# Kernel tuning notes

Measured on AMD Instinct MI355X. Metric: run time of the kernel, lower is better.

## Reference

```python
import jax, jax.numpy as jnp
import numpy as np

N, E, F_IN, HID, HEADS, NCLS, NG = 50000, 800000, 128, 128, 4, 10, 512
C = HID // HEADS          # per-head channels
BN_EPS = 1e-5
NEG_SLOPE = 0.2           # SuperGATConv default negative_slope
N_CONV = 3


def setup_inputs() -> dict:
    key = jax.random.key(0)
    ks = jax.random.split(key, 16)
    x = jax.random.normal(ks[0], (N, F_IN), jnp.float32)
    # edges with no self loops (reference appends self loops itself, as SuperGATConv does)
    src = jax.random.randint(ks[1], (E,), 0, N, dtype=jnp.int32)
    off = jax.random.randint(ks[2], (E,), 1, N, dtype=jnp.int32)
    dst = (src + off) % N
    edge_index = jnp.stack([src, dst], axis=0)
    batch = jnp.sort(jax.random.randint(ks[3], (N,), 0, NG, dtype=jnp.int32))
    s = 0.1
    # BatchNorm params per module init: weight=1, bias=1e-4 (running stats fresh: mean=0, var=1)
    inp = {
        "x": x, "edge_index": edge_index, "batch": batch,
        "bn_feat_g": jnp.ones((F_IN,), jnp.float32), "bn_feat_b": jnp.full((F_IN,), 1e-4, jnp.float32),
        "w_feat": jax.random.normal(ks[4], (F_IN, HID), jnp.float32) * s,
        "b_feat": jnp.zeros((HID,), jnp.float32),
        "bn_conv_g": jnp.ones((N_CONV, HID), jnp.float32), "bn_conv_b": jnp.full((N_CONV, HID), 1e-4, jnp.float32),
        "w_gat": jax.random.normal(ks[5], (N_CONV, HID, HID), jnp.float32) * s,
        "att_l": jax.random.normal(ks[6], (N_CONV, HEADS, C), jnp.float32) * s,
        "att_r": jax.random.normal(ks[7], (N_CONV, HEADS, C), jnp.float32) * s,
        "b_gat": jnp.zeros((N_CONV, HID), jnp.float32),
        "bn_fc_g": jnp.ones((HID,), jnp.float32), "bn_fc_b": jnp.full((HID,), 1e-4, jnp.float32),
        "w_fc": jax.random.normal(ks[8], (HID, HID), jnp.float32) * s,
        "b_fc": jnp.zeros((HID,), jnp.float32),
        "bn_hid_g": jnp.ones((HID,), jnp.float32), "bn_hid_b": jnp.full((HID,), 1e-4, jnp.float32),
        "w_cls": jax.random.normal(ks[9], (HID, NCLS), jnp.float32) * s,
        "b_cls": jnp.zeros((NCLS,), jnp.float32),
    }
    return inp


def _bn_eval(h, g, b):
    # eval-mode BatchNorm1d with fresh running stats (mean=0, var=1)
    return h * (g / jnp.sqrt(1.0 + BN_EPS)) + b


def _segment_softmax(a, seg, num_segments):
    # softmax over edges grouped by destination node (PyG softmax semantics)
    m = jax.ops.segment_max(a, seg, num_segments=num_segments)
    a = jnp.exp(a - m[seg])
    s = jax.ops.segment_sum(a, seg, num_segments=num_segments)
    return a / (s[seg] + 1e-16)


def _supergat_mx(h, src, dst, W, att_l, att_r, bias):
    # h: [N, HID] -> per-head features [N, H, C]
    hh = (h @ W).reshape(N, HEADS, C)
    h_j = hh[src]  # source (message) features  [E2, H, C]
    h_i = hh[dst]  # destination features       [E2, H, C]
    logits = jnp.einsum('ehc,ehc->eh', h_i, h_j)                       # MX dot-product
    alpha = jnp.einsum('ehc,hc->eh', h_j, att_l) + jnp.einsum('ehc,hc->eh', h_i, att_r)
    alpha = alpha * jax.nn.sigmoid(logits)
    alpha = jax.nn.leaky_relu(alpha, NEG_SLOPE)
    alpha = _segment_softmax(alpha, dst, N)                            # [E2, H]
    out = jax.ops.segment_sum(h_j * alpha[..., None], dst, num_segments=N)
    return out.reshape(N, HID) + bias


def reference(x, edge_index, batch, bn_feat_g, bn_feat_b, w_feat, b_feat,
              bn_conv_g, bn_conv_b, w_gat, att_l, att_r, b_gat,
              bn_fc_g, bn_fc_b, w_fc, b_fc, bn_hid_g, bn_hid_b, w_cls, b_cls):
    loops = jnp.arange(N, dtype=edge_index.dtype)
    src = jnp.concatenate([edge_index[0], loops])   # SuperGATConv adds self loops
    dst = jnp.concatenate([edge_index[1], loops])
    h = _bn_eval(x, bn_feat_g, bn_feat_b)
    h = jax.nn.relu(h @ w_feat + b_feat)            # GCNConv(gfn=True) == Linear
    for i in range(N_CONV):
        h = _bn_eval(h, bn_conv_g[i], bn_conv_b[i])
        h = jax.nn.relu(_supergat_mx(h, src, dst, w_gat[i], att_l[i], att_r[i], b_gat[i]))
    g = jax.ops.segment_sum(h, batch, num_segments=NG)  # global_add_pool -> [NG, HID]
    g = _bn_eval(g, bn_fc_g, bn_fc_b)
    g = jax.nn.relu(g @ w_fc + b_fc)
    g = _bn_eval(g, bn_hid_g, bn_hid_b)
    logits = g @ w_cls + b_cls
    att_loss = jnp.float32(0.0)  # eval mode: no edge-sampled attention loss
    return jax.nn.log_softmax(logits, axis=-1), att_loss
```

## Files before the change

### kernel.cpp

```cpp
#include <hip/hip_runtime.h>

#define NN 50000
#define EE 800000
#define FHID 128
#define NHEAD 4
#define NGRAPH 512
#define NCLS 10
#define BK 256
#define BCH 2048
#define NBLK_E 391
#define NBUCK 196
#define CAPB 6144

typedef unsigned short u16;
typedef unsigned int u32;
typedef unsigned long long u64;
typedef __attribute__((ext_vector_type(8))) short bf16x8;
typedef __attribute__((ext_vector_type(4))) float f32x4;
typedef __attribute__((ext_vector_type(2))) float f32x2;

__device__ __forceinline__ float bf2f(u16 u){
    union { u32 i; float f; } v; v.i = ((u32)u) << 16; return v.f;
}
__device__ __forceinline__ float bflo(u32 u){
    union { u32 i; float f; } v; v.i = u << 16; return v.f;
}
__device__ __forceinline__ float bfhi(u32 u){
    union { u32 i; float f; } v; v.i = u & 0xffff0000u; return v.f;
}
__device__ __forceinline__ u16 f2bf(float f){
    union { float f; u32 i; } v; v.f = f;
    u32 r = v.i + 0x7fffu + ((v.i >> 16) & 1u);
    return (u16)(r >> 16);
}
__device__ __forceinline__ u32 pack2(float a, float b){
    return ((u32)f2bf(b) << 16) | f2bf(a);
}
__device__ __forceinline__ float loadF(const void* p, int i, int isf32){
    return isf32 ? ((const float*)p)[i] : bf2f(((const u16*)p)[i]);
}
__device__ __forceinline__ void unpk8(uint4 v, float* f){
    f[0]=bflo(v.x); f[1]=bfhi(v.x);
    f[2]=bflo(v.y); f[3]=bfhi(v.y);
    f[4]=bflo(v.z); f[5]=bfhi(v.z);
    f[6]=bflo(v.w); f[7]=bfhi(v.w);
}
__device__ __forceinline__ void unpk8v(uint4 v, f32x2* h){
    h[0] = (f32x2){bflo(v.x), bfhi(v.x)};
    h[1] = (f32x2){bflo(v.y), bfhi(v.y)};
    h[2] = (f32x2){bflo(v.z), bfhi(v.z)};
    h[3] = (f32x2){bflo(v.w), bfhi(v.w)};
}

__device__ __forceinline__ float quad_red(float x){
    int t0 = __builtin_amdgcn_mov_dpp(__float_as_int(x), 0xB1, 0xF, 0xF, true);
    float y = x + __int_as_float(t0);
    int t1 = __builtin_amdgcn_mov_dpp(__float_as_int(y), 0x4E, 0xF, 0xF, true);
    return y + __int_as_float(t1);
}

__device__ int detect_local(const u16* x, int tid, int nthreads, int* lds){
    int ok = 0;
    for (int i = tid; i < 1024; i += nthreads){
        u16 u = x[i];
        int e = (u >> 7) & 0xFF;
        if ((u & 0x7fff) == 0 || (e >= 0x70 && e <= 0x85)) ok++;
    }
    lds[tid] = ok;
    __syncthreads();
    for (int o2 = nthreads >> 1; o2 > 0; o2 >>= 1){
        if (tid < o2) lds[tid] += lds[tid + o2];
        __syncthreads();
    }
    int r = (lds[0] < 900) ? 1 : 0;
    __syncthreads();
    return r;
}

__global__ __launch_bounds__(256) void prep_all(
        const u16* __restrict__ xz,
        const void* w_feat, const void* b_feat, const void* bn_feat_g, const void* bn_feat_b,
        const void* w_gat, const void* bn_conv_g, const void* bn_conv_b, const void* b_gat,
        const void* wfc, const void* bfc, const void* bnfg, const void* bnfb,
        const void* bnhg, const void* bnhb, const void* wcls, const void* bcls,
        const void* attl, const void* attr,
        u16* __restrict__ Wt, float* __restrict__ cvec, float* __restrict__ biasv,
        float* __restrict__ hp, int* __restrict__ dflag, int* __restrict__ gcur)
{
    __shared__ int ldsi[256];
    __shared__ float red[128];
    int bid = blockIdx.x, t = threadIdx.x;
    int isf32 = detect_local(xz, t, 256, ldsi);
    if (bid == 0){
        if (t == 0) dflag[0] = isf32;
        gcur[t] = t * CAPB;
    }

    if (bid < 512){
        if (t >= 128) return;
        int L = bid >> 7;
        int n = bid & 127;
        int k = t;
        const float rs = rsqrtf(1.0f + 1e-5f);
        float wv, bg, bb;
        if (L == 0){
            wv = loadF(w_feat, k*FHID + n, isf32);
            bg = loadF(bn_feat_g, k, isf32);
            bb = loadF(bn_feat_b, k, isf32);
        } else {
            wv = loadF(w_gat, (L-1)*FHID*FHID + k*FHID + n, isf32);
            bg = loadF(bn_conv_g, (L-1)*FHID + k, isf32);
            bb = loadF(bn_conv_b, (L-1)*FHID + k, isf32);
        }
        Wt[L*FHID*FHID + n*FHID + k] = f2bf(bg * rs * wv);
        red[k] = bb * wv;
        __syncthreads();
        for (int o2 = 64; o2 > 0; o2 >>= 1){
            if (k < o2) red[k] += red[k + o2];
            __syncthreads();
        }
        if (k == 0){
            float c = red[0];
            if (L == 0) c += loadF(b_feat, n, isf32);
            cvec[L*FHID + n] = c;
            if (L > 0) biasv[L*FHID + n] = loadF(b_gat, (L-1)*FHID + n, isf32);
        }
    } else {
        int gt = (bid - 512)*256 + t;
        for (int i = gt; i < FHID*FHID; i += 16*256) hp[i] = loadF(wfc, i, isf32);
        if (gt < FHID*NCLS) hp[16384 + gt] = loadF(wcls, gt, isf32);
        if (gt >= 2048 && gt < 2048 + 3*FHID){
            int i = gt - 2048;
            hp[18320 + i] = loadF(attl, i, isf32);
            hp[18704 + i] = loadF(attr, i, isf32);
        }
        if (gt >= 2560 && gt < 2560 + FHID){
            int tt = gt - 2560;
            hp[17664 + tt] = loadF(bnfg, tt, isf32);
            hp[17792 + tt] = loadF(bnfb, tt, isf32);
            hp[17920 + tt] = loadF(bfc,  tt, isf32);
            hp[18048 + tt] = loadF(bnhg, tt, isf32);
            hp[18176 + tt] = loadF(bnhb, tt, isf32);
        }
        if (gt >= 3072 && gt < 3072 + NCLS) hp[18304 + (gt - 3072)] = loadF(bcls, gt - 3072, isf32);
    }
}

__global__ __launch_bounds__(256) void gemm128(const void* __restrict__ A,
                                               const u16* __restrict__ Wt,
                                               const float* __restrict__ cvec,
                                               u16* __restrict__ out, int relu,
                                               int araw, const int* __restrict__ flag,
                                               const float* __restrict__ attl,
                                               const float* __restrict__ attr,
                                               float* __restrict__ al,
                                               float* __restrict__ ar)
{
    int wave = threadIdx.x >> 6;
    int lane = threadIdx.x & 63;
    int m = lane & 15, quad = lane >> 4;
    int row = blockIdx.x * 64 + wave * 16 + m;
    bool v0 = row < NN;
    bool f32in = araw && flag[0];
    const u16*  Au = (const u16*)A;
    const float* Af = (const float*)A;
    f32x4 acc[8];
#pragma unroll
    for (int j = 0; j < 8; j++) acc[j] = (f32x4){0.f,0.f,0.f,0.f};
#pragma unroll
    for (int t = 0; t < 4; t++){
        bf16x8 a0 = {0,0,0,0,0,0,0,0};
        int kof = t*32 + quad*8;
        if (f32in){
            if (v0){
                const float* p = Af + (size_t)row*FHID + kof;
                float4 u0 = *(const float4*)p, u1 = *(const float4*)(p+4);
                a0[0]=(short)f2bf(u0.x); a0[1]=(short)f2bf(u0.y);
                a0[2]=(short)f2bf(u0.z); a0[3]=(short)f2bf(u0.w);
                a0[4]=(short)f2bf(u1.x); a0[5]=(short)f2bf(u1.y);
                a0[6]=(short)f2bf(u1.z); a0[7]=(short)f2bf(u1.w);
            }
        } else {
            if (v0) a0 = *(const bf16x8*)(Au + (size_t)row*FHID + kof);
        }
#pragma unroll
        for (int ct = 0; ct < 8; ct++){
            bf16x8 wfrag = *(const bf16x8*)(Wt + (ct*16 + m)*FHID + kof);
            acc[ct] = __builtin_amdgcn_mfma_f32_16x16x32_bf16(wfrag, a0, acc[ct], 0, 0, 0);
        }
    }
    bool doa = (attl != nullptr);
    float sl[4] = {0.f,0.f,0.f,0.f};
    float sr[4] = {0.f,0.f,0.f,0.f};
#pragma unroll
    for (int ct = 0; ct < 8; ct++){
        int cb = ct*16 + quad*4;
        float4 cv = *(const float4*)(cvec + cb);
        float w0 = acc[ct][0] + cv.x;
        float w1 = acc[ct][1] + cv.y;
        float w2 = acc[ct][2] + cv.z;
        float w3 = acc[ct][3] + cv.w;
        if (relu){
            w0 = fmaxf(w0, 0.f); w1 = fmaxf(w1, 0.f);
            w2 = fmaxf(w2, 0.f); w3 = fmaxf(w3, 0.f);
        }
        if (doa){
            int h = ct >> 1;
            float4 tl = *(const float4*)(attl + cb);
            float4 tr = *(const float4*)(attr + cb);
            sl[h] += w0*tl.x + w1*tl.y + w2*tl.z + w3*tl.w;
            sr[h] += w0*tr.x + w1*tr.y + w2*tr.z + w3*tr.w;
        }
        if (v0){
            uint2 st; st.x = pack2(w0, w1); st.y = pack2(w2, w3);
            *(uint2*)(out + (size_t)row*FHID + cb) = st;
        }
    }
    if (doa){
#pragma unroll
        for (int h = 0; h < 4; h++){
            sl[h] += __shfl_xor(sl[h], 16, 64);
            sl[h] += __shfl_xor(sl[h], 32, 64);
            sr[h] += __shfl_xor(sr[h], 16, 64);
            sr[h] += __shfl_xor(sr[h], 32, 64);
        }
        if (v0){
            al[row*NHEAD + quad] = sl[quad];
            ar[row*NHEAD + quad] = sr[quad];
        }
    }
}

__global__ __launch_bounds__(256) void bin_edges(const int* __restrict__ srcp,
        const int* __restrict__ dstp, int* __restrict__ gcur, u64* __restrict__ binned)
{
    __shared__ int h[BK], lb[BK], gb[BK], cur[BK];
    __shared__ u64 stage[BCH];
    int t = threadIdx.x;
    h[t] = 0;
    __syncthreads();
    int base = blockIdx.x * BCH;
    int sv[8], dv[8];
#pragma unroll
    for (int k = 0; k < 8; k++){
        int e = base + k*256 + t;
        int d = -1, s = 0;
        if (e < EE){
            d = dstp[e]; s = srcp[e];
            if ((u32)d >= NN) d = -1;
        }
        sv[k] = s; dv[k] = d;
        if (d >= 0) atomicAdd(&h[d >> 8], 1);
    }
    __syncthreads();
    lb[t] = h[t];
    __syncthreads();
    for (int off = 1; off < BK; off <<= 1){
        int x = (t >= off) ? lb[t - off] : 0;
        __syncthreads();
        lb[t] += x;
        __syncthreads();
    }
    int excl = lb[t] - h[t];
    int tot  = lb[BK-1];
    __syncthreads();
    lb[t] = excl;
    gb[t] = h[t] ? atomicAdd(&gcur[t], h[t]) : 0;
    cur[t] = 0;
    __syncthreads();
#pragma unroll
    for (int k = 0; k < 8; k++){
        int d = dv[k];
        if (d >= 0){
            int b = d >> 8;
            int p = lb[b] + atomicAdd(&cur[b], 1);
            stage[p] = ((u64)(u32)d << 32) | (u32)sv[k];
        }
    }
    __syncthreads();
    for (int i = t; i < tot; i += 256){
        u64 pr = stage[i];
        int b = (int)(pr >> 40);
        binned[gb[b] + (i - lb[b])] = pr;
    }
}

__global__ __launch_bounds__(512) void build_csr(const u64* __restrict__ binned,
        const int* __restrict__ gcur, int2* __restrict__ rowdeg, int* __restrict__ colbuf)
{
    __shared__ int deg[BK], ls[BK], cur[BK];
    __shared__ int colstage[CAPB];
    int b = blockIdx.x, t = threadIdx.x;
    int gb = b * CAPB;
    int cnt = gcur[b] - gb;
    if (cnt < 0) cnt = 0;
    if (cnt > CAPB) cnt = CAPB;
    if (t < BK) deg[t] = 0;
    __syncthreads();
    for (int i = t; i < cnt; i += 512){
        int d = (int)(binned[gb + i] >> 32);
        atomicAdd(&deg[d & 255], 1);
    }
    __syncthreads();
    if (t < BK) ls[t] = deg[t];
    __syncthreads();
    for (int off = 1; off < BK; off <<= 1){
        int x = (t < BK && t >= off) ? ls[t - off] : 0;
        __syncthreads();
        if (t < BK) ls[t] += x;
        __syncthreads();
    }
    if (t < BK){
        int excl = ls[t] - deg[t];
        int node = b*256 + t;
        if (node < NN) rowdeg[node] = (int2){gb + excl, gb + excl + deg[t]};
        cur[t] = excl;
    }
    __syncthreads();
    for (int i = t; i < cnt; i += 512){
        u64 pr = binned[gb + i];
        int d = (int)(pr >> 32) & 255;
        int s = (int)(u32)pr;
        int p = atomicAdd(&cur[d], 1);
        colstage[p] = s;
    }
    __syncthreads();
    for (int i = t; i < cnt; i += 512) colbuf[gb + i] = colstage[i];
}

__device__ __forceinline__ void load_e(uint4& X, float& F, int e, int e1,
        const int* __restrict__ colbuf, const u16* __restrict__ hh,
        const float* __restrict__ al, int chbase, int head)
{
    int si = colbuf[e];
    bool bad = (e >= e1) || ((u32)si >= NN);
    if (bad) si = 0;
    X = *(const uint4*)(hh + (size_t)si*FHID + chbase);
    float f = al[si*NHEAD + head];
    F = bad ? -1e30f : f;
}

__device__ __forceinline__ void comp_e(uint4 X, float F,
        const f32x2* hd2, float arn, float& s, f32x2* o2)
{
    f32x2 hs2[4]; unpk8v(X, hs2);
    f32x2 d2 = hd2[0]*hs2[0];
    d2 = hd2[1]*hs2[1] + d2;
    d2 = hd2[2]*hs2[2] + d2;
    d2 = hd2[3]*hs2[3] + d2;
    float lg = quad_red(d2[0] + d2[1]);
    float a2 = (F + arn) * (1.0f / (1.0f + __expf(-lg)));
    a2 = fmaxf(a2, 0.2f*a2);
    float pe = __expf(fminf(a2, 60.f));
    s += pe;
    f32x2 pe2 = (f32x2){pe, pe};
    o2[0] = pe2*hs2[0] + o2[0];
    o2[1] = pe2*hs2[1] + o2[1];
    o2[2] = pe2*hs2[2] + o2[2];
    o2[3] = pe2*hs2[3] + o2[3];
}

__global__ __launch_bounds__(256, 8) void supergat_conv(const u16* __restrict__ hh,
        const float* __restrict__ al, const float* __restrict__ ar,
        const int2* __restrict__ rowdeg, const int* __restrict__ colbuf,
        const float* __restrict__ bias, u16* __restrict__ hout)
{
    int node = (blockIdx.x*256 + threadIdx.x) >> 6;
    int lane = threadIdx.x & 63;
    int group = lane >> 4;
    int gl    = lane & 15;
    int head  = gl >> 2;
    int chbase = head*32 + (gl & 3)*8;
    if (node >= NN) return;

    uint4 hdv = *(const uint4*)(hh + (size_t)node*FHID + chbase);
    f32x2 hd2[4]; unpk8v(hdv, hd2);
    float arn = ar[node*NHEAD + head];
    float aln = al[node*NHEAD + head];

    f32x2 dd2 = hd2[0]*hd2[0];
    dd2 = hd2[1]*hd2[1] + dd2;
    dd2 = hd2[2]*hd2[2] + dd2;
    dd2 = hd2[3]*hd2[3] + dd2;
    float d = quad_red(dd2[0] + dd2[1]);
    float a = (aln + arn) * (1.0f / (1.0f + __expf(-d)));
    a = fmaxf(a, 0.2f*a);
    float p = __expf(fminf(a, 60.f));
    if (group != 0) p = 0.f;
    float s = p;
    f32x2 p2 = (f32x2){p, p};
    f32x2 o2[4];
    o2[0] = p2*hd2[0];
    o2[1] = p2*hd2[1];
    o2[2] = p2*hd2[2];
    o2[3] = p2*hd2[3];

    int2 rd = rowdeg[node];
    int e0 = rd.x, e1 = rd.y;
    if (e0 < 0) e0 = 0;
    if (e1 > BK*CAPB) e1 = BK*CAPB;
    int it = (e1 - e0 + 3) >> 2;
    int e = e0 + group;

    if (it > 0){
        uint4 xA, xB; float fA, fB;
        load_e(xA, fA, e, e1, colbuf, hh, al, chbase, head);
        e += 4;
        while (true){
            if (it == 1){ comp_e(xA, fA, hd2, arn, s, o2); break; }
            load_e(xB, fB, e, e1, colbuf, hh, al, chbase, head); e += 4;
            comp_e(xA, fA, hd2, arn, s, o2);
            --it;
            if (it == 1){ comp_e(xB, fB, hd2, arn, s, o2); break; }
            load_e(xA, fA, e, e1, colbuf, hh, al, chbase, head); e += 4;
            comp_e(xB, fB, hd2, arn, s, o2);
            --it;
        }
    }

    s += __shfl_xor(s, 16, 64);
    s += __shfl_xor(s, 32, 64);
#pragma unroll
    for (int i = 0; i < 4; i++){
        float x0 = o2[i][0], x1 = o2[i][1];
        x0 += __shfl_xor(x0, 16, 64);
        x0 += __shfl_xor(x0, 32, 64);
        x1 += __shfl_xor(x1, 16, 64);
        x1 += __shfl_xor(x1, 32, 64);
        o2[i] = (f32x2){x0, x1};
    }

    if (group == 0){
        float inv = 1.0f / (s + 1e-16f);
        uint4 w;
        w.x = pack2(fmaxf(o2[0][0]*inv + bias[chbase+0], 0.f),
                    fmaxf(o2[0][1]*inv + bias[chbase+1], 0.f));
        w.y = pack2(fmaxf(o2[1][0]*inv + bias[chbase+2], 0.f),
                    fmaxf(o2[1][1]*inv + bias[chbase+3], 0.f));
        w.z = pack2(fmaxf(o2[2][0]*inv + bias[chbase+4], 0.f),
                    fmaxf(o2[2][1]*inv + bias[chbase+5], 0.f));
        w.w = pack2(fmaxf(o2[3][0]*inv + bias[chbase+6], 0.f),
                    fmaxf(o2[3][1]*inv + bias[chbase+7], 0.f));
        *(uint4*)(hout + (size_t)node*FHID + chbase) = w;
    }
}

__global__ void pool_head(const u16* __restrict__ h, const int* __restrict__ batch,
                          const float* __restrict__ hp, const int* __restrict__ flag,
                          void* __restrict__ out)
{
    __shared__ int bounds[2];
    __shared__ float gb[FHID];
    __shared__ float g2[FHID];
    __shared__ float lg[16];
    int gi = blockIdx.x, t = threadIdx.x;
    int isf32 = flag[0];
    if (t < 2){
        int target = gi + t;
        int lo = 0, hi = NN;
        while (lo < hi){
            int mid = (lo + hi) >> 1;
            if (batch[mid] < target) lo = mid + 1; else hi = mid;
        }
        bounds[t] = lo;
    }
    __syncthreads();
    float s0 = 0.f, s1 = 0.f, s2 = 0.f, s3 = 0.f;
    int node = bounds[0], nend = bounds[1];
    for (; node + 3 < nend; node += 4){
        s0 += bf2f(h[(size_t)(node+0)*FHID + t]);
        s1 += bf2f(h[(size_t)(node+1)*FHID + t]);
        s2 += bf2f(h[(size_t)(node+2)*FHID + t]);
        s3 += bf2f(h[(size_t)(node+3)*FHID + t]);
    }
    for (; node < nend; node++) s0 += bf2f(h[(size_t)node*FHID + t]);
    float acc0 = (s0 + s1) + (s2 + s3);
    const float rs = rsqrtf(1.0f + 1e-5f);
    gb[t] = acc0 * (hp[17664 + t] * rs) + hp[17792 + t];
    __syncthreads();
    float acc = hp[17920 + t];
    for (int k = 0; k < FHID; k++) acc += gb[k] * hp[k*FHID + t];
    acc = fmaxf(acc, 0.f);
    g2[t] = acc * (hp[18048 + t] * rs) + hp[18176 + t];
    __syncthreads();
    if (t < NCLS){
        float l = hp[18304 + t];
        for (int k = 0; k < FHID; k++) l += g2[k] * hp[16384 + k*NCLS + t];
        lg[t] = l;
    }
    __syncthreads();
    if (t == 0){
        float mx = lg[0];
        for (int j = 1; j < NCLS; j++) mx = fmaxf(mx, lg[j]);
        float se = 0.f;
        for (int j = 0; j < NCLS; j++) se += __expf(lg[j] - mx);
        float lse = logf(se) + mx;
        if (isf32){
            float* o = (float*)out;
            for (int j = 0; j < NCLS; j++) o[gi*NCLS + j] = lg[j] - lse;
            if (gi == 0) o[NGRAPH*NCLS] = 0.f;
        } else {
            u16* o = (u16*)out;
            for (int j = 0; j < NCLS; j++) o[gi*NCLS + j] = f2bf(lg[j] - lse);
            if (gi == 0) o[NGRAPH*NCLS] = 0;
        }
    }
}

extern "C" void kernel_launch(void* const* d_in, const int* in_sizes, int n_in,
                              void* d_out, int out_size, void* d_ws, size_t ws_size,
                              hipStream_t stream)
{
    (void)in_sizes; (void)n_in; (void)out_size; (void)ws_size;
    const void* x         = d_in[0];
    const int* edge       = (const int*)d_in[1];
    const int* batch      = (const int*)d_in[2];

    char* ws = (char*)d_ws;
    size_t off = 0;
    auto alloc = [&](size_t bytes) -> char* {
        char* p = ws + off; off += (bytes + 255) & ~(size_t)255; return p;
    };
    int*   dflag   = (int*)  alloc(256);
    u16*   WtAll   = (u16*)  alloc((size_t)4*FHID*FHID*2);
    float* cvecAll = (float*)alloc((size_t)4*FHID*4);
    float* biasv   = (float*)alloc((size_t)4*FHID*4);
    float* headp   = (float*)alloc((size_t)19088*4);
    float* al      = (float*)alloc((size_t)NN*NHEAD*4);
    float* ar      = (float*)alloc((size_t)NN*NHEAD*4);
    int*   gcur    = (int*)  alloc((size_t)BK*4);
    int2*  rowdeg  = (int2*) alloc((size_t)NN*8);
    int*   colbuf  = (int*)  alloc((size_t)(BK*CAPB + 64)*4);
    u16*   hA      = (u16*)  alloc((size_t)NN*FHID*2);
    u16*   hB      = (u16*)  alloc((size_t)NN*FHID*2);
    u64*   binned  = (u64*)hB;

    const int* srcp = edge;
    const int* dstp = edge + EE;

    prep_all<<<528, 256, 0, stream>>>((const u16*)x,
        d_in[5], d_in[6], d_in[3], d_in[4], d_in[9], d_in[7], d_in[8], d_in[12],
        d_in[15], d_in[16], d_in[13], d_in[14], d_in[17], d_in[18], d_in[19], d_in[20],
        d_in[10], d_in[11],
        WtAll, cvecAll, biasv, headp, dflag, gcur);

    bin_edges<<<NBLK_E, 256, 0, stream>>>(srcp, dstp, gcur, binned);
    build_csr<<<NBUCK, 512, 0, stream>>>(binned, gcur, rowdeg, colbuf);

    gemm128<<<(NN + 63)/64, 256, 0, stream>>>(x, WtAll, cvecAll, hA, 1, 1, dflag,
                                              nullptr, nullptr, nullptr, nullptr);

    for (int i = 0; i < 3; i++){
        gemm128<<<(NN + 63)/64, 256, 0, stream>>>(hA, WtAll + (i+1)*FHID*FHID,
                                                  cvecAll + (i+1)*FHID, hB, 0, 0, dflag,
                                                  headp + 18320 + i*FHID,
                                                  headp + 18704 + i*FHID, al, ar);
        supergat_conv<<<(NN + 3)/4, 256, 0, stream>>>(hB, al, ar, rowdeg, colbuf,
                                                      biasv + (i+1)*FHID, hA);
    }

    pool_head<<<NGRAPH, 128, 0, stream>>>(hA, batch, headp, dflag, d_out);
}
```

Before: 380.8 us.

## Merge prep with edge binning and CSR build with first GEMM; widen pool head

Independent stages now share one launch each. Parameter prep and edge binning run as one grid, split by block index. CSR construction and the first feature GEMM also run as one grid. The gcur bucket cursors are now zeroed with a memset, so binning no longer waits for prep. The pooling/head kernel moves to 512 threads, splitting the node sum and the FC matvec across four sub-groups. This cuts launch count and fills idle CUs during small serial stages, at the cost of higher shared-memory use per block in the merged kernels.

```diff
diff --git a/kernel.cpp b/kernel.cpp
--- a/kernel.cpp
+++ b/kernel.cpp
@@ -11,6 +11,7 @@
 #define NBLK_E 391
 #define NBUCK 196
 #define CAPB 6144
+#define NBLK_G 782
 
 typedef unsigned short u16;
 typedef unsigned int u32;
@@ -39,12 +40,6 @@
 __device__ __forceinline__ float loadF(const void* p, int i, int isf32){
     return isf32 ? ((const float*)p)[i] : bf2f(((const u16*)p)[i]);
 }
-__device__ __forceinline__ void unpk8(uint4 v, float* f){
-    f[0]=bflo(v.x); f[1]=bfhi(v.x);
-    f[2]=bflo(v.y); f[3]=bfhi(v.y);
-    f[4]=bflo(v.z); f[5]=bfhi(v.z);
-    f[6]=bflo(v.w); f[7]=bfhi(v.w);
-}
 __device__ __forceinline__ void unpk8v(uint4 v, f32x2* h){
     h[0] = (f32x2){bflo(v.x), bfhi(v.x)};
     h[1] = (f32x2){bflo(v.y), bfhi(v.y)};
@@ -77,7 +72,7 @@
     return r;
 }
 
-__global__ __launch_bounds__(256) void prep_all(
+__device__ __forceinline__ void prep_body(int bid, int t,
         const u16* __restrict__ xz,
         const void* w_feat, const void* b_feat, const void* bn_feat_g, const void* bn_feat_b,
         const void* w_gat, const void* bn_conv_g, const void* bn_conv_b, const void* b_gat,
@@ -85,16 +80,12 @@
         const void* bnhg, const void* bnhb, const void* wcls, const void* bcls,
         const void* attl, const void* attr,
         u16* __restrict__ Wt, float* __restrict__ cvec, float* __restrict__ biasv,
-        float* __restrict__ hp, int* __restrict__ dflag, int* __restrict__ gcur)
+        float* __restrict__ hp, int* __restrict__ dflag)
 {
     __shared__ int ldsi[256];
     __shared__ float red[128];
-    int bid = blockIdx.x, t = threadIdx.x;
     int isf32 = detect_local(xz, t, 256, ldsi);
-    if (bid == 0){
-        if (t == 0) dflag[0] = isf32;
-        gcur[t] = t * CAPB;
-    }
+    if (bid == 0 && t == 0) dflag[0] = isf32;
 
     if (bid < 512){
         if (t >= 128) return;
@@ -146,20 +137,92 @@
     }
 }
 
-__global__ __launch_bounds__(256) void gemm128(const void* __restrict__ A,
-                                               const u16* __restrict__ Wt,
-                                               const float* __restrict__ cvec,
-                                               u16* __restrict__ out, int relu,
-                                               int araw, const int* __restrict__ flag,
-                                               const float* __restrict__ attl,
-                                               const float* __restrict__ attr,
-                                               float* __restrict__ al,
-                                               float* __restrict__ ar)
-{
-    int wave = threadIdx.x >> 6;
-    int lane = threadIdx.x & 63;
+__device__ __forceinline__ void bin_body(int bid, int t,
+        const int* __restrict__ srcp, const int* __restrict__ dstp,
+        int* __restrict__ gcur, u64* __restrict__ binned)
+{
+    __shared__ int h[BK], lb[BK], gbs[BK], cur[BK];
+    __shared__ u64 stage[BCH];
+    h[t] = 0;
+    __syncthreads();
+    int base = bid * BCH;
+    int sv[8], dv[8];
+#pragma unroll
+    for (int k = 0; k < 8; k++){
+        int e = base + k*256 + t;
+        int d = -1, s = 0;
+        if (e < EE){
+            d = dstp[e]; s = srcp[e];
+            if ((u32)d >= NN) d = -1;
+        }
+        sv[k] = s; dv[k] = d;
+        if (d >= 0) atomicAdd(&h[d >> 8], 1);
+    }
+    __syncthreads();
+    lb[t] = h[t];
+    __syncthreads();
+    for (int off = 1; off < BK; off <<= 1){
+        int x = (t >= off) ? lb[t - off] : 0;
+        __syncthreads();
+        lb[t] += x;
+        __syncthreads();
+    }
+    int excl = lb[t] - h[t];
+    int tot  = lb[BK-1];
+    __syncthreads();
+    lb[t] = excl;
+    gbs[t] = t*CAPB + (h[t] ? atomicAdd(&gcur[t], h[t]) : 0);
+    cur[t] = 0;
+    __syncthreads();
+#pragma unroll
+    for (int k = 0; k < 8; k++){
+        int d = dv[k];
+        if (d >= 0){
+            int b = d >> 8;
+            int p = lb[b] + atomicAdd(&cur[b], 1);
+            stage[p] = ((u64)(u32)d << 32) | (u32)sv[k];
+        }
+    }
+    __syncthreads();
+    for (int i = t; i < tot; i += 256){
+        u64 pr = stage[i];
+        int b = (int)(pr >> 40);
+        binned[gbs[b] + (i - lb[b])] = pr;
+    }
+}
+
+__global__ __launch_bounds__(256) void prep_bin(
+        const u16* __restrict__ xz,
+        const void* w_feat, const void* b_feat, const void* bn_feat_g, const void* bn_feat_b,
+        const void* w_gat, const void* bn_conv_g, const void* bn_conv_b, const void* b_gat,
+        const void* wfc, const void* bfc, const void* bnfg, const void* bnfb,
+        const void* bnhg, const void* bnhb, const void* wcls, const void* bcls,
+        const void* attl, const void* attr,
+        u16* __restrict__ Wt, float* __restrict__ cvec, float* __restrict__ biasv,
+        float* __restrict__ hp, int* __restrict__ dflag,
+        const int* __restrict__ srcp, const int* __restrict__ dstp,
+        int* __restrict__ gcur, u64* __restrict__ binned)
+{
+    if (blockIdx.x < 528){
+        prep_body(blockIdx.x, threadIdx.x, xz, w_feat, b_feat, bn_feat_g, bn_feat_b,
+                  w_gat, bn_conv_g, bn_conv_b, b_gat, wfc, bfc, bnfg, bnfb,
+                  bnhg, bnhb, wcls, bcls, attl, attr, Wt, cvec, biasv, hp, dflag);
+    } else {
+        bin_body(blockIdx.x - 528, threadIdx.x, srcp, dstp, gcur, binned);
+    }
+}
+
+__device__ __forceinline__ void gemm_body(int bid, int tid,
+        const void* __restrict__ A, const u16* __restrict__ Wt,
+        const float* __restrict__ cvec, u16* __restrict__ out, int relu,
+        int araw, const int* __restrict__ flag,
+        const float* __restrict__ attl, const float* __restrict__ attr,
+        float* __restrict__ al, float* __restrict__ ar)
+{
+    int wave = tid >> 6;
+    int lane = tid & 63;
     int m = lane & 15, quad = lane >> 4;
-    int row = blockIdx.x * 64 + wave * 16 + m;
+    int row = bid * 64 + wave * 16 + m;
     bool v0 = row < NN;
     bool f32in = araw && flag[0];
     const u16*  Au = (const u16*)A;
@@ -231,93 +294,46 @@
     }
 }
 
-__global__ __launch_bounds__(256) void bin_edges(const int* __restrict__ srcp,
-        const int* __restrict__ dstp, int* __restrict__ gcur, u64* __restrict__ binned)
-{
-    __shared__ int h[BK], lb[BK], gb[BK], cur[BK];
-    __shared__ u64 stage[BCH];
-    int t = threadIdx.x;
-    h[t] = 0;
-    __syncthreads();
-    int base = blockIdx.x * BCH;
-    int sv[8], dv[8];
-#pragma unroll
-    for (int k = 0; k < 8; k++){
-        int e = base + k*256 + t;
-        int d = -1, s = 0;
-        if (e < EE){
-            d = dstp[e]; s = srcp[e];
-            if ((u32)d >= NN) d = -1;
-        }
-        sv[k] = s; dv[k] = d;
-        if (d >= 0) atomicAdd(&h[d >> 8], 1);
-    }
-    __syncthreads();
-    lb[t] = h[t];
-    __syncthreads();
-    for (int off = 1; off < BK; off <<= 1){
-        int x = (t >= off) ? lb[t - off] : 0;
-        __syncthreads();
-        lb[t] += x;
-        __syncthreads();
-    }
-    int excl = lb[t] - h[t];
-    int tot  = lb[BK-1];
-    __syncthreads();
-    lb[t] = excl;
-    gb[t] = h[t] ? atomicAdd(&gcur[t], h[t]) : 0;
-    cur[t] = 0;
-    __syncthreads();
-#pragma unroll
-    for (int k = 0; k < 8; k++){
-        int d = dv[k];
-        if (d >= 0){
-            int b = d >> 8;
-            int p = lb[b] + atomicAdd(&cur[b], 1);
-            stage[p] = ((u64)(u32)d << 32) | (u32)sv[k];
-        }
-    }
-    __syncthreads();
-    for (int i = t; i < tot; i += 256){
-        u64 pr = stage[i];
-        int b = (int)(pr >> 40);
-        binned[gb[b] + (i - lb[b])] = pr;
-    }
-}
-
-__global__ __launch_bounds__(512) void build_csr(const u64* __restrict__ binned,
+__global__ __launch_bounds__(256) void gemm128(const void* __restrict__ A,
+        const u16* __restrict__ Wt, const float* __restrict__ cvec,
+        u16* __restrict__ out, int relu, int araw, const int* __restrict__ flag,
+        const float* __restrict__ attl, const float* __restrict__ attr,
+        float* __restrict__ al, float* __restrict__ ar)
+{
+    gemm_body(blockIdx.x, threadIdx.x, A, Wt, cvec, out, relu, araw, flag,
+              attl, attr, al, ar);
+}
+
+__device__ __forceinline__ void csr_body(int b, int t, const u64* __restrict__ binned,
         const int* __restrict__ gcur, int2* __restrict__ rowdeg, int* __restrict__ colbuf)
 {
     __shared__ int deg[BK], ls[BK], cur[BK];
     __shared__ int colstage[CAPB];
-    int b = blockIdx.x, t = threadIdx.x;
     int gb = b * CAPB;
-    int cnt = gcur[b] - gb;
+    int cnt = gcur[b];
     if (cnt < 0) cnt = 0;
     if (cnt > CAPB) cnt = CAPB;
-    if (t < BK) deg[t] = 0;
-    __syncthreads();
-    for (int i = t; i < cnt; i += 512){
+    deg[t] = 0;
+    __syncthreads();
+    for (int i = t; i < cnt; i += 256){
         int d = (int)(binned[gb + i] >> 32);
         atomicAdd(&deg[d & 255], 1);
     }
     __syncthreads();
-    if (t < BK) ls[t] = deg[t];
+    ls[t] = deg[t];
     __syncthreads();
     for (int off = 1; off < BK; off <<= 1){
-        int x = (t < BK && t >= off) ? ls[t - off] : 0;
+        int x = (t >= off) ? ls[t - off] : 0;
         __syncthreads();
-        if (t < BK) ls[t] += x;
+        ls[t] += x;
         __syncthreads();
     }
-    if (t < BK){
-        int excl = ls[t] - deg[t];
-        int node = b*256 + t;
-        if (node < NN) rowdeg[node] = (int2){gb + excl, gb + excl + deg[t]};
-        cur[t] = excl;
-    }
-    __syncthreads();
-    for (int i = t; i < cnt; i += 512){
+    int excl = ls[t] - deg[t];
+    int node = b*256 + t;
+    if (node < NN) rowdeg[node] = (int2){gb + excl, gb + excl + deg[t]};
+    cur[t] = excl;
+    __syncthreads();
+    for (int i = t; i < cnt; i += 256){
         u64 pr = binned[gb + i];
         int d = (int)(pr >> 32) & 255;
         int s = (int)(u32)pr;
@@ -325,7 +341,21 @@
         colstage[p] = s;
     }
     __syncthreads();
-    for (int i = t; i < cnt; i += 512) colbuf[gb + i] = colstage[i];
+    for (int i = t; i < cnt; i += 256) colbuf[gb + i] = colstage[i];
+}
+
+__global__ __launch_bounds__(256) void csr_gemm(const u64* __restrict__ binned,
+        const int* __restrict__ gcur, int2* __restrict__ rowdeg, int* __restrict__ colbuf,
+        const void* __restrict__ A, const u16* __restrict__ Wt,
+        const float* __restrict__ cvec, u16* __restrict__ out,
+        const int* __restrict__ flag)
+{
+    if (blockIdx.x < NBUCK){
+        csr_body(blockIdx.x, threadIdx.x, binned, gcur, rowdeg, colbuf);
+    } else {
+        gemm_body(blockIdx.x - NBUCK, threadIdx.x, A, Wt, cvec, out, 1, 1, flag,
+                  nullptr, nullptr, nullptr, nullptr);
+    }
 }
 
 __device__ __forceinline__ void load_e(uint4& X, float& F, int e, int e1,
@@ -445,15 +475,17 @@
     }
 }
 
-__global__ void pool_head(const u16* __restrict__ h, const int* __restrict__ batch,
-                          const float* __restrict__ hp, const int* __restrict__ flag,
-                          void* __restrict__ out)
+__global__ __launch_bounds__(512) void pool_head(const u16* __restrict__ h,
+        const int* __restrict__ batch, const float* __restrict__ hp,
+        const int* __restrict__ flag, void* __restrict__ out)
 {
     __shared__ int bounds[2];
+    __shared__ float part[4][FHID];
     __shared__ float gb[FHID];
     __shared__ float g2[FHID];
     __shared__ float lg[16];
     int gi = blockIdx.x, t = threadIdx.x;
+    int ch = t & 127, sub = t >> 7;
     int isf32 = flag[0];
     if (t < 2){
         int target = gi + t;
@@ -465,23 +497,34 @@
         bounds[t] = lo;
     }
     __syncthreads();
-    float s0 = 0.f, s1 = 0.f, s2 = 0.f, s3 = 0.f;
-    int node = bounds[0], nend = bounds[1];
-    for (; node + 3 < nend; node += 4){
-        s0 += bf2f(h[(size_t)(node+0)*FHID + t]);
-        s1 += bf2f(h[(size_t)(node+1)*FHID + t]);
-        s2 += bf2f(h[(size_t)(node+2)*FHID + t]);
-        s3 += bf2f(h[(size_t)(node+3)*FHID + t]);
-    }
-    for (; node < nend; node++) s0 += bf2f(h[(size_t)node*FHID + t]);
-    float acc0 = (s0 + s1) + (s2 + s3);
+    float s0 = 0.f, s1 = 0.f;
+    int node = bounds[0] + sub, nend = bounds[1];
+    for (; node + 4 < nend; node += 8){
+        s0 += bf2f(h[(size_t)(node  )*FHID + ch]);
+        s1 += bf2f(h[(size_t)(node+4)*FHID + ch]);
+    }
+    for (; node < nend; node += 4) s0 += bf2f(h[(size_t)node*FHID + ch]);
+    part[sub][ch] = s0 + s1;
+    __syncthreads();
     const float rs = rsqrtf(1.0f + 1e-5f);
-    gb[t] = acc0 * (hp[17664 + t] * rs) + hp[17792 + t];
-    __syncthreads();
-    float acc = hp[17920 + t];
-    for (int k = 0; k < FHID; k++) acc += gb[k] * hp[k*FHID + t];
-    acc = fmaxf(acc, 0.f);
-    g2[t] = acc * (hp[18048 + t] * rs) + hp[18176 + t];
+    if (t < FHID){
+        float acc0 = (part[0][t] + part[1][t]) + (part[2][t] + part[3][t]);
+        gb[t] = acc0 * (hp[17664 + t] * rs) + hp[17792 + t];
+    }
+    __syncthreads();
+    {
+        float acc = 0.f;
+        int k0 = sub*32;
+        for (int k = k0; k < k0 + 32; k++) acc += gb[k] * hp[k*FHID + ch];
+        __syncthreads();
+        part[sub][ch] = acc;
+    }
+    __syncthreads();
+    if (t < FHID){
+        float acc = hp[17920 + t] + (part[0][t] + part[1][t]) + (part[2][t] + part[3][t]);
+        acc = fmaxf(acc, 0.f);
+        g2[t] = acc * (hp[18048 + t] * rs) + hp[18176 + t];
+    }
     __syncthreads();
     if (t < NCLS){
         float l = hp[18304 + t];
@@ -538,26 +581,25 @@
     const int* srcp = edge;
     const int* dstp = edge + EE;
 
-    prep_all<<<528, 256, 0, stream>>>((const u16*)x,
+    hipMemsetAsync(gcur, 0, (size_t)BK*4, stream);
+
+    prep_bin<<<528 + NBLK_E, 256, 0, stream>>>((const u16*)x,
         d_in[5], d_in[6], d_in[3], d_in[4], d_in[9], d_in[7], d_in[8], d_in[12],
         d_in[15], d_in[16], d_in[13], d_in[14], d_in[17], d_in[18], d_in[19], d_in[20],
         d_in[10], d_in[11],
-        WtAll, cvecAll, biasv, headp, dflag, gcur);
-
-    bin_edges<<<NBLK_E, 256, 0, stream>>>(srcp, dstp, gcur, binned);
-    build_csr<<<NBUCK, 512, 0, stream>>>(binned, gcur, rowdeg, colbuf);
-
-    gemm128<<<(NN + 63)/64, 256, 0, stream>>>(x, WtAll, cvecAll, hA, 1, 1, dflag,
-                                              nullptr, nullptr, nullptr, nullptr);
+        WtAll, cvecAll, biasv, headp, dflag, srcp, dstp, gcur, binned);
+
+    csr_gemm<<<NBUCK + NBLK_G, 256, 0, stream>>>(binned, gcur, rowdeg, colbuf,
+                                                 x, WtAll, cvecAll, hA, dflag);
 
     for (int i = 0; i < 3; i++){
-        gemm128<<<(NN + 63)/64, 256, 0, stream>>>(hA, WtAll + (i+1)*FHID*FHID,
-                                                  cvecAll + (i+1)*FHID, hB, 0, 0, dflag,
-                                                  headp + 18320 + i*FHID,
-                                                  headp + 18704 + i*FHID, al, ar);
+        gemm128<<<NBLK_G, 256, 0, stream>>>(hA, WtAll + (i+1)*FHID*FHID,
+                                            cvecAll + (i+1)*FHID, hB, 0, 0, dflag,
+                                            headp + 18320 + i*FHID,
+                                            headp + 18704 + i*FHID, al, ar);
         supergat_conv<<<(NN + 3)/4, 256, 0, stream>>>(hB, al, ar, rowdeg, colbuf,
                                                       biasv + (i+1)*FHID, hA);
     }
 
-    pool_head<<<NGRAPH, 128, 0, stream>>>(hA, batch, headp, dflag, d_out);
-}
+    pool_head<<<NGRAPH, 512, 0, stream>>>(hA, batch, headp, dflag, d_out);
+}
```

New measurement: 364.3 us. 4.4% less time.
